# Kernel optimization log

Hardware: AMD Instinct MI355X
Metric: run time of the kernel (lower is better)

Reference implementation:

```python
import jax, jax.numpy as jnp
import numpy as np

# Model dims: E experts, T total routed tokens, D model dim, H expert hidden dim
E, T, D, H = 8, 16384, 2048, 5632


def setup_inputs() -> dict:
    key = jax.random.key(0)
    k1, k2, k3, k4 = jax.random.split(key, 4)
    init_std = 0.02
    x = jax.random.normal(k1, (T, D), dtype=jnp.float32)
    # w1/w3: (num_experts, hidden_dim, dim); w2: (num_experts, dim, hidden_dim)
    w1 = jax.random.normal(k2, (E, H, D), dtype=jnp.float32) * init_std
    w2 = jax.random.normal(k3, (E, D, H), dtype=jnp.float32) * init_std
    w3 = jax.random.normal(k4, (E, H, D), dtype=jnp.float32) * init_std
    # Tokens are pre-sorted by expert; even split so sum == T (no padding path)
    num_tokens_per_expert = jnp.full((E,), T // E, dtype=jnp.int32)
    return {"x": x, "w1": w1, "w2": w2, "w3": w3,
            "num_tokens_per_expert": num_tokens_per_expert}


def reference(x, w1, w2, w3, num_tokens_per_expert):
    """Grouped-GEMM SwiGLU experts: out[t] = silu(x@w1[e].T) * (x@w3[e].T) @ w2[e].T
    where e is the expert owning token t (tokens sorted by expert).
    lax.ragged_dot is the exact grouped-GEMM primitive: lhs (m,k), rhs (g,k,n),
    group_sizes (g,) -> (m,n). Weights are stored as (g, out, in), so swap to (g, in, out),
    matching the torch matmul with transpose(-2, -1).
    """
    groups = num_tokens_per_expert.astype(jnp.int32)
    gate = jax.lax.ragged_dot(x, jnp.swapaxes(w1, 1, 2), groups)   # (T, H)
    up = jax.lax.ragged_dot(x, jnp.swapaxes(w3, 1, 2), groups)     # (T, H)
    h = jax.nn.silu(gate) * up                                      # fused SwiGLU
    out = jax.lax.ragged_dot(h, jnp.swapaxes(w2, 1, 2), groups)    # (T, D)
    return out
```

## Files before the change

kernel.cpp:

```cpp
#include <hip/hip_runtime.h>
#include <hip/hip_bf16.h>


typedef __bf16 bf16x8 __attribute__((ext_vector_type(8)));
typedef float f32x4 __attribute__((ext_vector_type(4)));
typedef unsigned short u16x8 __attribute__((ext_vector_type(8)));

constexpr int E = 8;
constexpr int T = 16384;
constexpr int D = 2048;
constexpr int H = 5632;

#define DEV static __device__ __forceinline__

DEV unsigned short f2bf(float f) {
    unsigned u = __builtin_bit_cast(unsigned, f);
    u = (u + 0x7FFFu + ((u >> 16) & 1u)) >> 16;
    return (unsigned short)u;
}

DEV void gload16(const void* g, void* l) {
    __builtin_amdgcn_global_load_lds(
        (const __attribute__((address_space(1))) void*)g,
        (__attribute__((address_space(3))) void*)l, 16, 0, 0);
}

DEV f32x4 mfma16(bf16x8 a, bf16x8 b, f32x4 c) {
    return __builtin_amdgcn_mfma_f32_16x16x32_bf16(a, b, c, 0, 0, 0);
}

__global__ __launch_bounds__(256) void k_cvt(const float* __restrict__ in,
                                             unsigned short* __restrict__ out,
                                             long n8) {
    long i = (long)blockIdx.x * blockDim.x + threadIdx.x;
    long stride = (long)gridDim.x * blockDim.x;
    for (; i < n8; i += stride) {
        const float4* p = (const float4*)(in + i * 8);
        float4 a = p[0], b = p[1];
        u16x8 r;
        r[0] = f2bf(a.x); r[1] = f2bf(a.y); r[2] = f2bf(a.z); r[3] = f2bf(a.w);
        r[4] = f2bf(b.x); r[5] = f2bf(b.y); r[6] = f2bf(b.z); r[7] = f2bf(b.w);
        *(u16x8*)(out + i * 8) = r;
    }
}

__global__ __launch_bounds__(256) void k_cvt_w13(
    const float* __restrict__ in, unsigned short* __restrict__ out,
    int which) {
    const long n8 = (long)E * H * D / 8;
    long i = (long)blockIdx.x * blockDim.x + threadIdx.x;
    long stride = (long)gridDim.x * blockDim.x;
    for (; i < n8; i += stride) {
        int col8 = (int)(i & 255);
        int row = (int)(i >> 8);
        int e = row / H;
        int h = row - e * H;
        int rr = ((h >> 4) << 5) + (which << 4) + (h & 15);
        const float4* p = (const float4*)(in + i * 8);
        float4 a = p[0], b = p[1];
        u16x8 r;
        r[0] = f2bf(a.x); r[1] = f2bf(a.y); r[2] = f2bf(a.z); r[3] = f2bf(a.w);
        r[4] = f2bf(b.x); r[5] = f2bf(b.y); r[6] = f2bf(b.z); r[7] = f2bf(b.w);
        *(u16x8*)(out + ((size_t)e * (2 * H) + rr) * D + (size_t)col8 * 8) = r;
    }
}

DEV int expert_of_row(const int* __restrict__ ntp, int row0) {
    int e = 0, s = 0;
    for (int i = 0; i < E; ++i) {
        int c = ntp[i];
        if (row0 < s + c) { e = i; break; }
        s += c;
    }
    return e;
}

template <int LDA, int LDB, int NT>
DEV void gemm_core(const unsigned short* pA,
                   const unsigned short* pB,
                   unsigned short* sA, unsigned short* sB, int tid,
                   f32x4 (&acc)[8][4]) {
    const int wid = tid >> 6, lane = tid & 63;
    const int ksl = (((lane >> 4) ^ (lane & 3) ^ ((lane >> 2) & 3)) << 3);
    const int frA = ((wid >> 2) << 7) + (lane & 15);
    const int frB = ((wid & 3) << 6) + (lane & 15);
    const int aoff = frA * 32 + ksl;
    const int boff = frB * 32 + ksl;
    char* ldsA = (char*)sA + wid * 1024;
    char* ldsB = (char*)sB + wid * 1024;

    auto stageA = [&](int t) {
        const unsigned short* g = pA + t * 32;
        char* l = ldsA + (t & 3) * 16384;
        gload16(g, l);
        gload16(g + (size_t)128 * LDA, l + 8192);
    };
    auto stageB = [&](int t) {
        const unsigned short* g = pB + t * 32;
        char* l = ldsB + (t & 3) * 16384;
        gload16(g, l);
        gload16(g + (size_t)128 * LDB, l + 8192);
    };

    stageA(0); stageB(0);
    stageA(1); stageB(1);
    stageA(2); stageB(2);

    for (int t = 0; t < NT; ++t) {
        const int slot = t & 3;
        if (t + 3 < NT) stageA(t + 3);
        const int rem = NT - 1 - t;
        if (rem >= 3)      asm volatile("s_waitcnt vmcnt(10)" ::: "memory");
        else if (rem == 2) asm volatile("s_waitcnt vmcnt(8)" ::: "memory");
        else if (rem == 1) asm volatile("s_waitcnt vmcnt(4)" ::: "memory");
        else               asm volatile("s_waitcnt vmcnt(0)" ::: "memory");
        __builtin_amdgcn_s_barrier();
        __builtin_amdgcn_sched_barrier(0);

        const unsigned short* A = sA + slot * 8192;
        const unsigned short* B = sB + slot * 8192;
        bf16x8 a[4], b[4];
#pragma unroll
        for (int i = 0; i < 4; ++i) a[i] = *(const bf16x8*)&A[aoff + i * 512];
#pragma unroll
        for (int i = 0; i < 4; ++i) b[i] = *(const bf16x8*)&B[boff + i * 512];
        if (t + 3 < NT) stageB(t + 3);
        __builtin_amdgcn_s_setprio(1);
#pragma unroll
        for (int mi = 0; mi < 4; ++mi)
#pragma unroll
            for (int ni = 0; ni < 4; ++ni)
                acc[mi][ni] = mfma16(a[mi], b[ni], acc[mi][ni]);
        __builtin_amdgcn_s_setprio(0);
        __builtin_amdgcn_s_barrier();
#pragma unroll
        for (int i = 0; i < 4; ++i)
            a[i] = *(const bf16x8*)&A[aoff + 2048 + i * 512];
        __builtin_amdgcn_s_setprio(1);
#pragma unroll
        for (int mi = 0; mi < 4; ++mi)
#pragma unroll
            for (int ni = 0; ni < 4; ++ni)
                acc[4 + mi][ni] = mfma16(a[mi], b[ni], acc[4 + mi][ni]);
        __builtin_amdgcn_s_setprio(0);
        __builtin_amdgcn_s_barrier();
    }
}

__global__ __launch_bounds__(512, 2) void k_gate_up(
    const unsigned short* __restrict__ xb,
    const unsigned short* __restrict__ w13b,
    const int* __restrict__ ntp,
    unsigned short* __restrict__ hbuf) {
    __shared__ unsigned short sA[4 * 8192];
    __shared__ unsigned short sB[4 * 8192];

    const int nwg = gridDim.x;
    const int cpx = nwg >> 3;
    const int bid = blockIdx.x;
    const int swz = (bid & 7) * cpx + (bid >> 3);
    const int tm = swz & 63;
    const int tn = swz >> 6;

    const int row0 = tm << 8;
    const int e = expert_of_row(ntp, row0);
    const int tid = threadIdx.x;

    const int srow = tid >> 2;
    const int sslot = (tid & 3) ^ ((tid >> 2) & 3) ^ ((tid >> 4) & 3);
    const unsigned short* pA = xb + (size_t)(row0 + srow) * D + sslot * 8;
    const unsigned short* pB = w13b + (size_t)e * (2 * H) * D +
                               (size_t)((tn << 8) + srow) * D + sslot * 8;

    f32x4 acc[8][4] = {};
    gemm_core<D, D, D / 32>(pA, pB, sA, sB, tid, acc);

    const int wid = tid >> 6, lane = tid & 63;
    const int wm = wid >> 2, wn = wid & 3;
    const int rbase = row0 + (wm << 7) + ((lane >> 4) << 2);
    const int cbase = ((tn << 3) + (wn << 1)) << 4;
#pragma unroll
    for (int mi = 0; mi < 8; ++mi)
#pragma unroll
        for (int pi = 0; pi < 2; ++pi) {
            f32x4 g = acc[mi][2 * pi], u = acc[mi][2 * pi + 1];
            const int hcol = cbase + (pi << 4) + (lane & 15);
#pragma unroll
            for (int j = 0; j < 4; ++j) {
                float gv = g[j];
                float hv = gv * u[j] / (1.f + __expf(-gv));
                hbuf[(size_t)(rbase + (mi << 4) + j) * H + hcol] = f2bf(hv);
            }
        }
}

__global__ __launch_bounds__(512, 2) void k_down(
    const unsigned short* __restrict__ hbuf,
    const unsigned short* __restrict__ w2b,
    const int* __restrict__ ntp,
    float* __restrict__ out) {
    __shared__ unsigned short sA[4 * 8192];
    __shared__ unsigned short sB[4 * 8192];

    const int nwg = gridDim.x;
    const int cpx = nwg >> 3;
    const int bid = blockIdx.x;
    const int swz = (bid & 7) * cpx + (bid >> 3);
    const int tm = swz & 63;
    const int tn = swz >> 6;

    const int row0 = tm << 8;
    const int e = expert_of_row(ntp, row0);
    const int tid = threadIdx.x;

    const int srow = tid >> 2;
    const int sslot = (tid & 3) ^ ((tid >> 2) & 3) ^ ((tid >> 4) & 3);
    const unsigned short* pA = hbuf + (size_t)(row0 + srow) * H + sslot * 8;
    const unsigned short* pB = w2b + (size_t)e * D * H +
                               (size_t)((tn << 8) + srow) * H + sslot * 8;

    f32x4 acc[8][4] = {};
    gemm_core<H, H, H / 32>(pA, pB, sA, sB, tid, acc);

    const int wid = tid >> 6, lane = tid & 63;
    const int wm = wid >> 2, wn = wid & 3;
    const int rbase = row0 + (wm << 7) + ((lane >> 4) << 2);
    const int cb = (tn << 8) + (wn << 6) + (lane & 15);
#pragma unroll
    for (int mi = 0; mi < 8; ++mi)
#pragma unroll
        for (int ni = 0; ni < 4; ++ni) {
            f32x4 c = acc[mi][ni];
#pragma unroll
            for (int j = 0; j < 4; ++j)
                out[(size_t)(rbase + (mi << 4) + j) * D + cb + (ni << 4)] =
                    c[j];
        }
}

extern "C" void kernel_launch(void* const* d_in, const int* in_sizes, int n_in,
                              void* d_out, int out_size, void* d_ws,
                              size_t ws_size, hipStream_t stream) {
    const float* x = (const float*)d_in[0];
    const float* w1 = (const float*)d_in[1];
    const float* w2 = (const float*)d_in[2];
    const float* w3 = (const float*)d_in[3];
    const int* ntp = (const int*)d_in[4];
    float* out = (float*)d_out;

    char* ws = (char*)d_ws;
    unsigned short* xb = (unsigned short*)(ws + 0);
    unsigned short* w13b = (unsigned short*)(ws + 67108864L);
    unsigned short* hbuf = (unsigned short*)(ws + 67108864L + 385875968L);
    unsigned short* w2b = w13b;

    k_cvt<<<2048, 256, 0, stream>>>(x, xb, (long)T * D / 8);
    k_cvt_w13<<<2048, 256, 0, stream>>>(w1, w13b, 0);
    k_cvt_w13<<<2048, 256, 0, stream>>>(w3, w13b, 1);

    k_gate_up<<<(T / 256) * (2 * H / 256), 512, 0, stream>>>(xb, w13b, ntp,
                                                             hbuf);

    k_cvt<<<2048, 256, 0, stream>>>(w2, w2b, (long)E * D * H / 8);

    k_down<<<(T / 256) * (D / 256), 512, 0, stream>>>(hbuf, w2b, ntp, out);
}
```

Measured before the change: 1.659 ms.

## Switch GEMMs to 32x32x16 MFMA with BK=64 pipeline and fused conversions

Replaces the 16x16x32 MFMA GEMM core with a 32x32x16 bf16 MFMA core that uses 64-wide K tiles, double-buffered LDS and a reworked interleaving of loads and barriers. It merges the x/w1/w3 conversion launches into one kernel and, when the workspace is large enough, converts w2 inside the gate/up kernel so the separate launch is skipped. It also changes the block-to-tile mapping in both GEMMs and the interleave width of the w1/w3 layout. The aim is fewer LDS reads per FLOP, fewer launches and better overlap, at the cost of more registers per thread and a dependence on workspace size.

```diff
diff --git a/kernel.cpp b/kernel.cpp
--- a/kernel.cpp
+++ b/kernel.cpp
@@ -3,7 +3,7 @@
 
 
 typedef __bf16 bf16x8 __attribute__((ext_vector_type(8)));
-typedef float f32x4 __attribute__((ext_vector_type(4)));
+typedef float f32x16 __attribute__((ext_vector_type(16)));
 typedef unsigned short u16x8 __attribute__((ext_vector_type(8)));
 
 constexpr int E = 8;
@@ -25,44 +25,25 @@
         (__attribute__((address_space(3))) void*)l, 16, 0, 0);
 }
 
-DEV f32x4 mfma16(bf16x8 a, bf16x8 b, f32x4 c) {
-    return __builtin_amdgcn_mfma_f32_16x16x32_bf16(a, b, c, 0, 0, 0);
-}
-
-__global__ __launch_bounds__(256) void k_cvt(const float* __restrict__ in,
-                                             unsigned short* __restrict__ out,
-                                             long n8) {
-    long i = (long)blockIdx.x * blockDim.x + threadIdx.x;
-    long stride = (long)gridDim.x * blockDim.x;
-    for (; i < n8; i += stride) {
-        const float4* p = (const float4*)(in + i * 8);
-        float4 a = p[0], b = p[1];
-        u16x8 r;
-        r[0] = f2bf(a.x); r[1] = f2bf(a.y); r[2] = f2bf(a.z); r[3] = f2bf(a.w);
-        r[4] = f2bf(b.x); r[5] = f2bf(b.y); r[6] = f2bf(b.z); r[7] = f2bf(b.w);
-        *(u16x8*)(out + i * 8) = r;
-    }
-}
-
-__global__ __launch_bounds__(256) void k_cvt_w13(
-    const float* __restrict__ in, unsigned short* __restrict__ out,
-    int which) {
-    const long n8 = (long)E * H * D / 8;
-    long i = (long)blockIdx.x * blockDim.x + threadIdx.x;
-    long stride = (long)gridDim.x * blockDim.x;
-    for (; i < n8; i += stride) {
-        int col8 = (int)(i & 255);
-        int row = (int)(i >> 8);
-        int e = row / H;
-        int h = row - e * H;
-        int rr = ((h >> 4) << 5) + (which << 4) + (h & 15);
-        const float4* p = (const float4*)(in + i * 8);
-        float4 a = p[0], b = p[1];
-        u16x8 r;
-        r[0] = f2bf(a.x); r[1] = f2bf(a.y); r[2] = f2bf(a.z); r[3] = f2bf(a.w);
-        r[4] = f2bf(b.x); r[5] = f2bf(b.y); r[6] = f2bf(b.z); r[7] = f2bf(b.w);
-        *(u16x8*)(out + ((size_t)e * (2 * H) + rr) * D + (size_t)col8 * 8) = r;
-    }
+DEV f32x16 mfma32(bf16x8 a, bf16x8 b, f32x16 c) {
+    return __builtin_amdgcn_mfma_f32_32x32x16_bf16(a, b, c, 0, 0, 0);
+}
+
+DEV void vm4() { asm volatile("s_waitcnt vmcnt(4)" ::: "memory"); }
+DEV void vm2() { asm volatile("s_waitcnt vmcnt(2)" ::: "memory"); }
+DEV void vm0() { asm volatile("s_waitcnt vmcnt(0)" ::: "memory"); }
+DEV void barsb() {
+    __builtin_amdgcn_s_barrier();
+    __builtin_amdgcn_sched_barrier(0);
+}
+
+DEV void cvt8(const float* src, unsigned short* dst) {
+    float4 a = *(const float4*)src;
+    float4 c = *(const float4*)(src + 4);
+    u16x8 r;
+    r[0] = f2bf(a.x); r[1] = f2bf(a.y); r[2] = f2bf(a.z); r[3] = f2bf(a.w);
+    r[4] = f2bf(c.x); r[5] = f2bf(c.y); r[6] = f2bf(c.z); r[7] = f2bf(c.w);
+    *(u16x8*)dst = r;
 }
 
 DEV int expert_of_row(const int* __restrict__ ntp, int row0) {
@@ -75,167 +56,234 @@
     return e;
 }
 
-template <int LDA, int LDB, int NT>
-DEV void gemm_core(const unsigned short* pA,
-                   const unsigned short* pB,
-                   unsigned short* sA, unsigned short* sB, int tid,
-                   f32x4 (&acc)[8][4]) {
-    const int wid = tid >> 6, lane = tid & 63;
-    const int ksl = (((lane >> 4) ^ (lane & 3) ^ ((lane >> 2) & 3)) << 3);
-    const int frA = ((wid >> 2) << 7) + (lane & 15);
-    const int frB = ((wid & 3) << 6) + (lane & 15);
-    const int aoff = frA * 32 + ksl;
-    const int boff = frB * 32 + ksl;
-    char* ldsA = (char*)sA + wid * 1024;
-    char* ldsB = (char*)sB + wid * 1024;
-
-    auto stageA = [&](int t) {
-        const unsigned short* g = pA + t * 32;
-        char* l = ldsA + (t & 3) * 16384;
-        gload16(g, l);
-        gload16(g + (size_t)128 * LDA, l + 8192);
-    };
-    auto stageB = [&](int t) {
-        const unsigned short* g = pB + t * 32;
-        char* l = ldsB + (t & 3) * 16384;
-        gload16(g, l);
-        gload16(g + (size_t)128 * LDB, l + 8192);
-    };
-
-    stageA(0); stageB(0);
-    stageA(1); stageB(1);
-    stageA(2); stageB(2);
-
-    for (int t = 0; t < NT; ++t) {
-        const int slot = t & 3;
-        if (t + 3 < NT) stageA(t + 3);
-        const int rem = NT - 1 - t;
-        if (rem >= 3)      asm volatile("s_waitcnt vmcnt(10)" ::: "memory");
-        else if (rem == 2) asm volatile("s_waitcnt vmcnt(8)" ::: "memory");
-        else if (rem == 1) asm volatile("s_waitcnt vmcnt(4)" ::: "memory");
-        else               asm volatile("s_waitcnt vmcnt(0)" ::: "memory");
-        __builtin_amdgcn_s_barrier();
-        __builtin_amdgcn_sched_barrier(0);
-
-        const unsigned short* A = sA + slot * 8192;
-        const unsigned short* B = sB + slot * 8192;
-        bf16x8 a[4], b[4];
-#pragma unroll
-        for (int i = 0; i < 4; ++i) a[i] = *(const bf16x8*)&A[aoff + i * 512];
-#pragma unroll
-        for (int i = 0; i < 4; ++i) b[i] = *(const bf16x8*)&B[boff + i * 512];
-        if (t + 3 < NT) stageB(t + 3);
-        __builtin_amdgcn_s_setprio(1);
-#pragma unroll
-        for (int mi = 0; mi < 4; ++mi)
-#pragma unroll
-            for (int ni = 0; ni < 4; ++ni)
-                acc[mi][ni] = mfma16(a[mi], b[ni], acc[mi][ni]);
+__global__ __launch_bounds__(256) void k_cvt_pre(
+    const float* __restrict__ x, const float* __restrict__ w1,
+    const float* __restrict__ w3, unsigned short* __restrict__ xb,
+    unsigned short* __restrict__ w13b) {
+    const int bid = blockIdx.x, tid = threadIdx.x;
+    if (bid < 512) {
+        const long n8 = (long)T * D / 8;
+        for (long i = (long)bid * 256 + tid; i < n8; i += 512L * 256)
+            cvt8(x + i * 8, xb + i * 8);
+    } else {
+        const float* src = (bid < 1408) ? w1 : w3;
+        const int which = (bid < 1408) ? 0 : 1;
+        const int b0 = (bid < 1408) ? 512 : 1408;
+        const long n8 = (long)E * H * D / 8;
+        for (long i = (long)(bid - b0) * 256 + tid; i < n8; i += 896L * 256) {
+            int col8 = (int)(i & 255);
+            int rowi = (int)(i >> 8);
+            int e = rowi / H;
+            int h = rowi - e * H;
+            int rr = ((h >> 5) << 6) + (which << 5) + (h & 31);
+            cvt8(src + i * 8,
+                 w13b + ((size_t)e * (2 * H) + rr) * D + (size_t)col8 * 8);
+        }
+    }
+}
+
+__global__ __launch_bounds__(256) void k_cvt(const float* __restrict__ in,
+                                             unsigned short* __restrict__ out,
+                                             long n8) {
+    long i = (long)blockIdx.x * blockDim.x + threadIdx.x;
+    long stride = (long)gridDim.x * blockDim.x;
+    for (; i < n8; i += stride) cvt8(in + i * 8, out + i * 8);
+}
+
+template <int LD, int NT>
+DEV void gemm32(const unsigned short* pa, const unsigned short* pb,
+                unsigned short* sA, unsigned short* sB, int tid,
+                f32x16 (&acc)[4][2]) {
+    const int lane = tid & 63, wid = tid >> 6;
+    const int wm = wid >> 2, wn = wid & 3;
+    const int hi5 = lane >> 5, l7 = lane & 7;
+    int slot[4];
+#pragma unroll
+    for (int kk = 0; kk < 4; ++kk) slot[kk] = ((kk * 2 + hi5) ^ l7) << 3;
+    const int arow = (wm * 128 + (lane & 31)) * 64;
+    const int brow = (wn * 64 + (lane & 31)) * 64;
+    char* ldsA = (char*)sA;
+    char* ldsB = (char*)sB;
+    const int dA = wid << 10;
+    const int dB = ((wid >> 2) << 13) + ((wid & 3) << 10);
+
+    bf16x8 aX[2][4], aY[2][4], b[4];
+
+    auto stA = [&](const unsigned short* g, int off) {
+        gload16(g, ldsA + off + dA);
+        gload16(g + (size_t)128 * LD, ldsA + off + dA + 16384);
+    };
+    auto stB = [&](const unsigned short* g, int off) {
+        gload16(g, ldsB + off + dB);
+        gload16(g + (size_t)128 * LD, ldsB + off + dB + 16384);
+    };
+    auto rdA = [&](bf16x8 (&dst)[2][4], int off) {
+#pragma unroll
+        for (int m = 0; m < 2; ++m)
+#pragma unroll
+            for (int kk = 0; kk < 4; ++kk)
+                dst[m][kk] =
+                    *(const bf16x8*)&sA[off + arow + m * 2048 + slot[kk]];
+    };
+    auto rdB = [&](int off, int half) {
+#pragma unroll
+        for (int kk = 0; kk < 4; ++kk)
+            b[kk] = *(const bf16x8*)&sB[off + brow + half * 2048 + slot[kk]];
+    };
+    auto mm = [&](bf16x8 (&A)[2][4], int mb, int n) {
+#pragma unroll
+        for (int m = 0; m < 2; ++m)
+#pragma unroll
+            for (int kk = 0; kk < 4; ++kk)
+                acc[mb + m][n] = mfma32(A[m][kk], b[kk], acc[mb + m][n]);
+    };
+
+    stA(pa, 0);
+    stB(pb, 0);
+    stA(pa + 64 * LD, 8192);
+    stB(pb + 32 * LD, 4096);
+    vm4();
+    __builtin_amdgcn_s_barrier();
+    rdA(aX, 0);
+    stA(pa + 64, 32768);
+
+    auto tile = [&](int cbW, int o1, int o2, bool steady, bool st2,
+                    bf16x8 (&A0)[2][4], bf16x8 (&A1)[2][4]) {
+        const int cbB = cbW << 1;
+        const int nbB = cbB ^ 32768;
+        if (steady) vm4(); else vm2();
+        rdB(cbW, 0);
+        if (steady) stB(pb + o1, nbB);
+        barsb();
+        __builtin_amdgcn_s_setprio(1); mm(A0, 0, 0);
         __builtin_amdgcn_s_setprio(0);
-        __builtin_amdgcn_s_barrier();
-#pragma unroll
-        for (int i = 0; i < 4; ++i)
-            a[i] = *(const bf16x8*)&A[aoff + 2048 + i * 512];
-        __builtin_amdgcn_s_setprio(1);
-#pragma unroll
-        for (int mi = 0; mi < 4; ++mi)
-#pragma unroll
-            for (int ni = 0; ni < 4; ++ni)
-                acc[4 + mi][ni] = mfma16(a[mi], b[ni], acc[4 + mi][ni]);
+        if (steady) vm4(); else vm0();
+        rdA(A1, cbW + 4096);
+        if (steady) stA(pa + o1 + 64 * LD, nbB + 8192);
+        barsb();
+        __builtin_amdgcn_s_setprio(1); mm(A1, 2, 0);
         __builtin_amdgcn_s_setprio(0);
-        __builtin_amdgcn_s_barrier();
+        if (steady) vm4();
+        rdB(cbW, 1);
+        if (steady) stB(pb + o1 + 32 * LD, nbB + 4096);
+        barsb();
+        __builtin_amdgcn_s_setprio(1); mm(A1, 2, 1);
+        __builtin_amdgcn_s_setprio(0);
+        if (steady) {
+            vm4();
+            rdA(A1, cbW ^ 16384);
+            if (st2) stA(pa + o2, cbB);
+            barsb();
+        }
+        __builtin_amdgcn_s_setprio(1); mm(A0, 0, 1);
+        __builtin_amdgcn_s_setprio(0);
+    };
+
+#pragma unroll 1
+    for (int kt = 0; kt < NT - 2; kt += 2) {
+        tile(0, 64, 128, true, true, aX, aY);
+        tile(16384, 128, 192, true, true, aY, aX);
+        pa += 128;
+        pb += 128;
     }
+    tile(0, 64, 128, true, false, aX, aY);
+    tile(16384, 0, 0, false, false, aY, aX);
 }
 
 __global__ __launch_bounds__(512, 2) void k_gate_up(
     const unsigned short* __restrict__ xb,
     const unsigned short* __restrict__ w13b,
-    const int* __restrict__ ntp,
-    unsigned short* __restrict__ hbuf) {
-    __shared__ unsigned short sA[4 * 8192];
-    __shared__ unsigned short sB[4 * 8192];
-
-    const int nwg = gridDim.x;
-    const int cpx = nwg >> 3;
+    const float* __restrict__ w2, unsigned short* __restrict__ w2b,
+    const int* __restrict__ ntp, unsigned short* __restrict__ hbuf) {
+    __shared__ unsigned short sA[2 * 16384];
+    __shared__ unsigned short sB[2 * 16384];
+
     const int bid = blockIdx.x;
-    const int swz = (bid & 7) * cpx + (bid >> 3);
-    const int tm = swz & 63;
-    const int tn = swz >> 6;
+    const int tid = threadIdx.x;
+
+    if (w2) {
+        const float* src = w2 + (size_t)bid * 32768;
+        unsigned short* dst = w2b + (size_t)bid * 32768;
+#pragma unroll
+        for (int it = 0; it < 8; ++it) {
+            int o = (it * 512 + tid) * 8;
+            cvt8(src + o, dst + o);
+        }
+        vm0();
+    }
+
+    const int eg = bid & 7;
+    const int tm = eg * 8 + ((bid >> 3) & 7);
+    const int tn = bid >> 6;
 
     const int row0 = tm << 8;
     const int e = expert_of_row(ntp, row0);
-    const int tid = threadIdx.x;
-
-    const int srow = tid >> 2;
-    const int sslot = (tid & 3) ^ ((tid >> 2) & 3) ^ ((tid >> 4) & 3);
-    const unsigned short* pA = xb + (size_t)(row0 + srow) * D + sslot * 8;
-    const unsigned short* pB = w13b + (size_t)e * (2 * H) * D +
-                               (size_t)((tn << 8) + srow) * D + sslot * 8;
-
-    f32x4 acc[8][4] = {};
-    gemm_core<D, D, D / 32>(pA, pB, sA, sB, tid, acc);
-
-    const int wid = tid >> 6, lane = tid & 63;
+    const int lane = tid & 63, wid = tid >> 6;
+
+    const int sra = tid >> 3;
+    const int sca = (tid & 7) ^ (sra & 7);
+    const unsigned short* pa = xb + (size_t)(row0 + sra) * D + sca * 8;
+    const int brw = ((wid >> 2) << 6) + ((wid & 3) << 3) + (lane >> 3);
+    const int scb = (lane & 7) ^ (lane >> 3);
+    const unsigned short* pb =
+        w13b + ((size_t)e * (2 * H) + (tn << 8) + brw) * D + scb * 8;
+
+    f32x16 acc[4][2] = {};
+    gemm32<D, D / 64>(pa, pb, sA, sB, tid, acc);
+
     const int wm = wid >> 2, wn = wid & 3;
-    const int rbase = row0 + (wm << 7) + ((lane >> 4) << 2);
-    const int cbase = ((tn << 3) + (wn << 1)) << 4;
-#pragma unroll
-    for (int mi = 0; mi < 8; ++mi)
-#pragma unroll
-        for (int pi = 0; pi < 2; ++pi) {
-            f32x4 g = acc[mi][2 * pi], u = acc[mi][2 * pi + 1];
-            const int hcol = cbase + (pi << 4) + (lane & 15);
-#pragma unroll
-            for (int j = 0; j < 4; ++j) {
-                float gv = g[j];
-                float hv = gv * u[j] / (1.f + __expf(-gv));
-                hbuf[(size_t)(rbase + (mi << 4) + j) * H + hcol] = f2bf(hv);
-            }
+    const int hc = ((tn << 2) + wn) * 32 + (lane & 31);
+    const int rb = row0 + wm * 128 + ((lane >> 5) << 2);
+#pragma unroll
+    for (int m = 0; m < 4; ++m)
+#pragma unroll
+        for (int r = 0; r < 16; ++r) {
+            float g = acc[m][0][r], u = acc[m][1][r];
+            float hv = g * u / (1.f + __expf(-g));
+            int row = rb + m * 32 + (r & 3) + ((r >> 2) << 3);
+            hbuf[(size_t)row * H + hc] = f2bf(hv);
         }
 }
 
 __global__ __launch_bounds__(512, 2) void k_down(
     const unsigned short* __restrict__ hbuf,
-    const unsigned short* __restrict__ w2b,
-    const int* __restrict__ ntp,
+    const unsigned short* __restrict__ w2b, const int* __restrict__ ntp,
     float* __restrict__ out) {
-    __shared__ unsigned short sA[4 * 8192];
-    __shared__ unsigned short sB[4 * 8192];
-
-    const int nwg = gridDim.x;
-    const int cpx = nwg >> 3;
+    __shared__ unsigned short sA[2 * 16384];
+    __shared__ unsigned short sB[2 * 16384];
+
     const int bid = blockIdx.x;
-    const int swz = (bid & 7) * cpx + (bid >> 3);
-    const int tm = swz & 63;
-    const int tn = swz >> 6;
+    const int tid = threadIdx.x;
+    const int tn = bid & 7;
+    const int tm = bid >> 3;
 
     const int row0 = tm << 8;
     const int e = expert_of_row(ntp, row0);
-    const int tid = threadIdx.x;
-
-    const int srow = tid >> 2;
-    const int sslot = (tid & 3) ^ ((tid >> 2) & 3) ^ ((tid >> 4) & 3);
-    const unsigned short* pA = hbuf + (size_t)(row0 + srow) * H + sslot * 8;
-    const unsigned short* pB = w2b + (size_t)e * D * H +
-                               (size_t)((tn << 8) + srow) * H + sslot * 8;
-
-    f32x4 acc[8][4] = {};
-    gemm_core<H, H, H / 32>(pA, pB, sA, sB, tid, acc);
-
-    const int wid = tid >> 6, lane = tid & 63;
+    const int lane = tid & 63, wid = tid >> 6;
+
+    const int sra = tid >> 3;
+    const int sca = (tid & 7) ^ (sra & 7);
+    const unsigned short* pa = hbuf + (size_t)(row0 + sra) * H + sca * 8;
+    const int brw = ((wid >> 2) << 6) + ((wid & 3) << 3) + (lane >> 3);
+    const int scb = (lane & 7) ^ (lane >> 3);
+    const unsigned short* pb =
+        w2b + ((size_t)e * D + (tn << 8) + brw) * H + scb * 8;
+
+    f32x16 acc[4][2] = {};
+    gemm32<H, H / 64>(pa, pb, sA, sB, tid, acc);
+
     const int wm = wid >> 2, wn = wid & 3;
-    const int rbase = row0 + (wm << 7) + ((lane >> 4) << 2);
-    const int cb = (tn << 8) + (wn << 6) + (lane & 15);
-#pragma unroll
-    for (int mi = 0; mi < 8; ++mi)
-#pragma unroll
-        for (int ni = 0; ni < 4; ++ni) {
-            f32x4 c = acc[mi][ni];
-#pragma unroll
-            for (int j = 0; j < 4; ++j)
-                out[(size_t)(rbase + (mi << 4) + j) * D + cb + (ni << 4)] =
-                    c[j];
-        }
+    const int dc = (tn << 8) + (wn << 6) + (lane & 31);
+    const int rb = row0 + wm * 128 + ((lane >> 5) << 2);
+#pragma unroll
+    for (int m = 0; m < 4; ++m)
+#pragma unroll
+        for (int n = 0; n < 2; ++n)
+#pragma unroll
+            for (int r = 0; r < 16; ++r) {
+                int row = rb + m * 32 + (r & 3) + ((r >> 2) << 3);
+                out[(size_t)row * D + dc + n * 32] = acc[m][n][r];
+            }
 }
 
 extern "C" void kernel_launch(void* const* d_in, const int* in_sizes, int n_in,
@@ -251,17 +299,18 @@
     char* ws = (char*)d_ws;
     unsigned short* xb = (unsigned short*)(ws + 0);
     unsigned short* w13b = (unsigned short*)(ws + 67108864L);
-    unsigned short* hbuf = (unsigned short*)(ws + 67108864L + 385875968L);
-    unsigned short* w2b = w13b;
-
-    k_cvt<<<2048, 256, 0, stream>>>(x, xb, (long)T * D / 8);
-    k_cvt_w13<<<2048, 256, 0, stream>>>(w1, w13b, 0);
-    k_cvt_w13<<<2048, 256, 0, stream>>>(w3, w13b, 1);
-
-    k_gate_up<<<(T / 256) * (2 * H / 256), 512, 0, stream>>>(xb, w13b, ntp,
-                                                             hbuf);
-
-    k_cvt<<<2048, 256, 0, stream>>>(w2, w2b, (long)E * D * H / 8);
+    unsigned short* hbuf = (unsigned short*)(ws + 436207616L);
+    const bool big = ws_size >= 805306368UL;
+    unsigned short* w2b =
+        big ? (unsigned short*)(ws + 620756992L) : w13b;
+
+    k_cvt_pre<<<2304, 256, 0, stream>>>(x, w1, w3, xb, w13b);
+
+    k_gate_up<<<(T / 256) * (2 * H / 256), 512, 0, stream>>>(
+        xb, w13b, big ? w2 : nullptr, big ? w2b : nullptr, ntp, hbuf);
+
+    if (!big)
+        k_cvt<<<2048, 256, 0, stream>>>(w2, w2b, (long)E * D * H / 8);
 
     k_down<<<(T / 256) * (D / 256), 512, 0, stream>>>(hbuf, w2b, ntp, out);
 }
```

New measurement: 1.588 ms. -4.3%, faster.
